# Kernel optimization log

Measured on AMD Instinct MI355X. Metric: run time of the kernel, lower is better.

## Reference

```python
import jax, jax.numpy as jnp
import numpy as np

D_MODEL = 512
NUM_HEADS = 8
D_K = D_MODEL // NUM_HEADS
SCALE = float(np.sqrt(D_K))


def setup_inputs() -> dict:
    key = jax.random.key(0)
    ks = jax.random.split(key, 11)
    B, S, D = 2, 4096, D_MODEL
    std = 1.0 / np.sqrt(D)
    return {
        "query": jax.random.normal(ks[0], (B, S, D), jnp.float32),
        "key": jax.random.normal(ks[1], (B, S, D), jnp.float32),
        "value": jax.random.normal(ks[2], (B, S, D), jnp.float32),
        "w_q": jax.random.normal(ks[3], (D, D), jnp.float32) * std,
        "b_q": jax.random.normal(ks[4], (D,), jnp.float32) * std,
        "w_k": jax.random.normal(ks[5], (D, D), jnp.float32) * std,
        "b_k": jax.random.normal(ks[6], (D,), jnp.float32) * std,
        "w_v": jax.random.normal(ks[7], (D, D), jnp.float32) * std,
        "b_v": jax.random.normal(ks[8], (D,), jnp.float32) * std,
        "w_o": jax.random.normal(ks[9], (D, D), jnp.float32) * std,
        "b_o": jax.random.normal(ks[10], (D,), jnp.float32) * std,
    }


def reference(query, key, value, w_q, b_q, w_k, b_k, w_v, b_v, w_o, b_o):
    B, S, D = query.shape
    H, Dk = NUM_HEADS, D_K
    # Linear projections (torch Linear: x @ W^T + b), split into heads -> [B,H,S,Dk]
    Q = (query @ w_q.T + b_q).reshape(B, S, H, Dk).transpose(0, 2, 1, 3)
    K = (key @ w_k.T + b_k).reshape(B, S, H, Dk).transpose(0, 2, 1, 3)
    V = (value @ w_v.T + b_v).reshape(B, S, H, Dk).transpose(0, 2, 1, 3)
    # [B,H,S,S] attention scores — intentionally materialized like the original
    scores = jnp.einsum("bhqd,bhkd->bhqk", Q, K) / SCALE
    attn = jax.nn.softmax(scores, axis=-1)  # dropout rate 0 in eval baseline
    attended = jnp.einsum("bhqk,bhkd->bhqd", attn, V)
    attended = attended.transpose(0, 2, 1, 3).reshape(B, S, D)
    return attended @ w_o.T + b_o
```

## Files before the change

kernel.cpp:

```cpp
#include <hip/hip_runtime.h>
#include <math.h>

#define D_MODEL 512
#define NHEADS 8
#define DK 64
#define BATCH 2
#define SEQ 4096
#define NSPLIT 2
#define NIT 32
#define ATTN_SCALE 0.18033688011112043f

typedef _Float16 half8 __attribute__((ext_vector_type(8)));
typedef _Float16 half4 __attribute__((ext_vector_type(4)));
typedef __fp16 pkhalf2 __attribute__((ext_vector_type(2)));
typedef float f32x4 __attribute__((ext_vector_type(4)));
typedef float f32x16 __attribute__((ext_vector_type(16)));

union Pk8 { _Float16 h[8]; uint4 u; };
union Pk4 { _Float16 h[4]; uint2 u; };
union Pkz { pkhalf2 h2[2]; uint2 u; };
union Un4 { uint2 u; _Float16 h[4]; };
union PFu { unsigned int u[4]; half8 h8; };

#if __has_builtin(__builtin_amdgcn_exp2f)
#define EXP2F __builtin_amdgcn_exp2f
#else
#define EXP2F exp2f
#endif

#define MFMA16(a, b, c) __builtin_amdgcn_mfma_f32_16x16x32_f16((a), (b), (c), 0, 0, 0)
#define MFMA32(a, b, c) __builtin_amdgcn_mfma_f32_32x32x16_f16((a), (b), (c), 0, 0, 0)

#define PLSWAP(x, y) asm volatile("v_permlane32_swap_b32 %0, %1" : "+v"(x), "+v"(y))

__device__ __forceinline__ unsigned int cvtpk(float a, float b) {
    union { pkhalf2 h; unsigned int u; } u_;
    u_.h = __builtin_amdgcn_cvt_pkrtz(a, b);
    return u_.u;
}

__device__ __forceinline__ void gload_lds16(const _Float16* g, _Float16* l) {
    __builtin_amdgcn_global_load_lds(
        (const __attribute__((address_space(1))) void*)g,
        (__attribute__((address_space(3))) void*)l, 16, 0, 0);
}

#define WBLK 256
__global__ __launch_bounds__(256)
void prep(const float* __restrict__ wq, const float* __restrict__ wk,
          const float* __restrict__ wv, const float* __restrict__ wo,
          _Float16* __restrict__ hq, _Float16* __restrict__ hk,
          _Float16* __restrict__ hv, _Float16* __restrict__ ho) {
    int gid = blockIdx.x;
    const int w = gid / WBLK;
    gid -= w * WBLK;
    const float* src = w == 0 ? wq : (w == 1 ? wk : (w == 2 ? wv : wo));
    _Float16* hi     = w == 0 ? hq : (w == 1 ? hk : (w == 2 ? hv : ho));
    const int i = (gid * 256 + threadIdx.x) * 4;
    float4 v = *(const float4*)(src + i);
    Pkz h;
    h.h2[0] = __builtin_amdgcn_cvt_pkrtz(v.x, v.y);
    h.h2[1] = __builtin_amdgcn_cvt_pkrtz(v.z, v.w);
    *(uint2*)(hi + i) = h.u;
}

__global__ __launch_bounds__(256)
void gemm_qkv(const float* __restrict__ Aq, const float* __restrict__ Ak,
              const float* __restrict__ Av,
              const _Float16* __restrict__ Whq, const _Float16* __restrict__ Whk,
              const _Float16* __restrict__ Whv,
              const float* __restrict__ bq, const float* __restrict__ bk,
              const float* __restrict__ bv,
              _Float16* __restrict__ Qf, _Float16* __restrict__ Kf,
              _Float16* __restrict__ Vtf) {
    const int z = blockIdx.z;
    const float*    A    = z == 0 ? Aq  : (z == 1 ? Ak  : Av);
    const _Float16* Wh   = z == 0 ? Whq : (z == 1 ? Whk : Whv);
    const float*    bias = z == 0 ? bq  : (z == 1 ? bk  : bv);

    __shared__ __align__(16) _Float16 sA[2][128 * 64];
    __shared__ __align__(16) _Float16 sW[2][128 * 64];

    const int t    = threadIdx.x;
    const int lane = t & 63, wave = t >> 6;
    const int col  = lane & 15, quad = lane >> 4;
    const int wm   = (wave & 1) * 64, wn = (wave >> 1) * 64;
    const int m0   = blockIdx.y * 128, n0 = blockIdx.x * 128;

    const int subrow = lane >> 3;
    const int schunk = ((lane & 7) ^ subrow) * 8;

    const float* aBase = A + (size_t)(m0 + wave * 32 + subrow) * 512 + schunk;

    float4 ar[4][2];
    #define LOAD_A(K0)                                                            \
        do {                                                                       \
            _Pragma("unroll")                                                      \
            for (int j = 0; j < 4; ++j) {                                          \
                const float* s = aBase + (size_t)(j * 8) * 512 + (K0);             \
                ar[j][0] = *(const float4*)s;                                      \
                ar[j][1] = *(const float4*)(s + 4);                                \
            }                                                                      \
        } while (0)
    #define WRITE_A(BUF)                                                           \
        do {                                                                       \
            _Pragma("unroll")                                                      \
            for (int j = 0; j < 4; ++j) {                                          \
                uint4 p;                                                           \
                p.x = cvtpk(ar[j][0].x, ar[j][0].y);                               \
                p.y = cvtpk(ar[j][0].z, ar[j][0].w);                               \
                p.z = cvtpk(ar[j][1].x, ar[j][1].y);                               \
                p.w = cvtpk(ar[j][1].z, ar[j][1].w);                               \
                *(uint4*)&sA[BUF][(wave * 32 + j * 8) * 64 + lane * 8] = p;        \
            }                                                                      \
        } while (0)
    #define STAGE_W(K0, BUF)                                                       \
        do {                                                                       \
            _Pragma("unroll")                                                      \
            for (int j = 0; j < 4; ++j) {                                          \
                const int rw = wave * 32 + j * 8;                                  \
                gload_lds16(Wh + (size_t)(n0 + rw + subrow) * 512 + (K0) + schunk, \
                            &sW[BUF][rw * 64]);                                    \
            }                                                                      \
        } while (0)

    f32x4 acc[4][4] = {};

    STAGE_W(0, 0);
    LOAD_A(0);
    WRITE_A(0);

    for (int ck = 0; ck < 8; ++ck) {
        const int cur = ck & 1;
        __syncthreads();
        if (ck + 1 < 8) {
            STAGE_W((ck + 1) * 64, cur ^ 1);
            LOAD_A((ck + 1) * 64);
        }

        #pragma unroll
        for (int kc = 0; kc < 2; ++kc) {
            const int pos = ((kc * 4 + quad) ^ (col & 7)) * 8;
            half8 af[4], wf[4];
            #pragma unroll
            for (int mt = 0; mt < 4; ++mt)
                af[mt] = *(const half8*)&sA[cur][(wm + mt * 16 + col) * 64 + pos];
            #pragma unroll
            for (int nt = 0; nt < 4; ++nt)
                wf[nt] = *(const half8*)&sW[cur][(wn + nt * 16 + col) * 64 + pos];
            #pragma unroll
            for (int mt = 0; mt < 4; ++mt)
                #pragma unroll
                for (int nt = 0; nt < 4; ++nt)
                    acc[mt][nt] = MFMA16(af[mt], wf[nt], acc[mt][nt]);
        }

        if (ck + 1 < 8) WRITE_A(cur ^ 1);
    }

    float bv4[4];
    #pragma unroll
    for (int nt = 0; nt < 4; ++nt) bv4[nt] = bias[n0 + wn + nt * 16 + col];

    if (z < 2) {
        _Float16* Out = z == 0 ? Qf : Kf;
        const float alpha = z == 0 ? ATTN_SCALE : 1.0f;
        #pragma unroll
        for (int mt = 0; mt < 4; ++mt) {
            const int m = m0 + wm + mt * 16 + quad * 4;
            #pragma unroll
            for (int nt = 0; nt < 4; ++nt) {
                const int n = n0 + wn + nt * 16 + col;
                #pragma unroll
                for (int r = 0; r < 4; ++r)
                    Out[(size_t)(m + r) * 512 + n] = (_Float16)((acc[mt][nt][r] + bv4[nt]) * alpha);
            }
        }
    } else {
        #pragma unroll
        for (int mt = 0; mt < 4; ++mt) {
            const int m = m0 + wm + mt * 16 + quad * 4;
            const int b = m >> 12, s = m & (SEQ - 1);
            #pragma unroll
            for (int nt = 0; nt < 4; ++nt) {
                const int n = n0 + wn + nt * 16 + col;
                const int hh = n >> 6, d = n & (DK - 1);
                Pk4 p;
                #pragma unroll
                for (int r = 0; r < 4; ++r)
                    p.h[r] = (_Float16)(acc[mt][nt][r] + bv4[nt]);
                *(uint2*)&Vtf[((size_t)((b * NHEADS + hh) * DK + d)) * SEQ + s] = p.u;
            }
        }
    }
}

__global__ __launch_bounds__(256, 2)
void attn_mfma(const _Float16* __restrict__ Qf, const _Float16* __restrict__ Kf,
               const _Float16* __restrict__ Vtf,
               _Float16* __restrict__ Op0, _Float16* __restrict__ Op1,
               float2* __restrict__ Ml) {
    __shared__ __align__(16) _Float16 sK[2][64 * 64];
    __shared__ __align__(16) _Float16 sV[2][64 * 64];

    const int t    = threadIdx.x;
    const int lane = t & 63;
    const int wave = t >> 6;
    const int l31  = lane & 31;
    const int g    = lane >> 5;

    const int strm = blockIdx.x;
    const int h  = strm & (NHEADS - 1);
    const int z  = strm >> 3;
    const int b  = z >> 1;
    const int sp = z & 1;
    const int q0 = blockIdx.y * 256;
    const int kBase = sp * (SEQ / NSPLIT);

    const size_t rowBase = (size_t)b * SEQ;
    const size_t vBase   = ((size_t)(b * NHEADS + h)) * DK * SEQ;

    const int subrow = lane >> 3;
    const int schunk = ((lane & 7) ^ subrow) * 8;
    const _Float16* kP[2];
    const _Float16* vP[2];
    #pragma unroll
    for (int j = 0; j < 2; ++j) {
        const int rw = wave * 16 + j * 8;
        kP[j] = Kf + (rowBase + kBase + rw + subrow) * 512 + h * 64 + schunk;
        vP[j] = Vtf + vBase + (size_t)(rw + subrow) * SEQ + kBase + schunk;
        gload_lds16(kP[j], &sK[0][rw * 64]);
        gload_lds16(vP[j], &sV[0][rw * 64]);
        kP[j] += 64 * 512;
        vP[j] += 64;
    }

    half8 qf[2][4];
    #pragma unroll
    for (int qt = 0; qt < 2; ++qt)
        #pragma unroll
        for (int kc = 0; kc < 4; ++kc)
            qf[qt][kc] = *(const half8*)(Qf +
                (rowBase + q0 + wave * 64 + qt * 32 + l31) * 512 +
                h * 64 + kc * 16 + g * 8);

    const int rs = l31 & 7;

    float m_r = 0.0f;
    f32x16 nbv = {};
    float l_r[2] = { 0.0f, 0.0f };
    f32x16 of[2][2] = {};

    for (int itp = 0; itp < NIT; itp += 2) {
        #pragma unroll
        for (int cur = 0; cur < 2; ++cur) {
            const int it = itp + cur;
            __syncthreads();
            if (it + 1 < NIT) {
                #pragma unroll
                for (int j = 0; j < 2; ++j) {
                    const int rw = wave * 16 + j * 8;
                    gload_lds16(kP[j], &sK[cur ^ 1][rw * 64]);
                    gload_lds16(vP[j], &sV[cur ^ 1][rw * 64]);
                    kP[j] += 64 * 512;
                    vP[j] += 64;
                }
            }

            #pragma unroll
            for (int kt = 0; kt < 2; ++kt) {
                f32x16 sf0, sf1;
                __builtin_amdgcn_s_setprio(1);
                #pragma unroll
                for (int kc = 0; kc < 4; ++kc) {
                    const int pos = ((kc * 2 + g) ^ rs) * 8;
                    half8 kf = *(const half8*)&sK[cur][(kt * 32 + l31) * 64 + pos];
                    sf0 = MFMA32(kf, qf[0][kc], kc == 0 ? nbv : sf0);
                    sf1 = MFMA32(kf, qf[1][kc], kc == 0 ? nbv : sf1);
                }
                __builtin_amdgcn_s_setprio(0);

                float lrs0 = 0.0f, lrs1 = 0.0f;
                #pragma unroll
                for (int j2 = 0; j2 < 16; ++j2) {
                    sf0[j2] = EXP2F(sf0[j2]);  lrs0 += sf0[j2];
                    sf1[j2] = EXP2F(sf1[j2]);  lrs1 += sf1[j2];
                }
                l_r[0] += lrs0;
                l_r[1] += lrs1;

                PFu pf0[2], pf1[2];
                #define MKPF(P, PF)                                                  \
                    do {                                                             \
                        unsigned int x1 = cvtpk(P[0], P[1]),  x2 = cvtpk(P[2], P[3]);\
                        unsigned int y1 = cvtpk(P[4], P[5]),  y2 = cvtpk(P[6], P[7]);\
                        PLSWAP(x1, y1); PLSWAP(x2, y2);                              \
                        PF[0].u[0] = x1; PF[0].u[1] = x2;                            \
                        PF[0].u[2] = y1; PF[0].u[3] = y2;                            \
                        unsigned int a1 = cvtpk(P[8], P[9]),  a2 = cvtpk(P[10], P[11]);\
                        unsigned int b1 = cvtpk(P[12], P[13]), b2 = cvtpk(P[14], P[15]);\
                        PLSWAP(a1, b1); PLSWAP(a2, b2);                              \
                        PF[1].u[0] = a1; PF[1].u[1] = a2;                            \
                        PF[1].u[2] = b1; PF[1].u[3] = b2;                            \
                    } while (0)
                MKPF(sf0, pf0);
                MKPF(sf1, pf1);
                #undef MKPF

                __builtin_amdgcn_s_setprio(1);
                #pragma unroll
                for (int ks2 = 0; ks2 < 2; ++ks2) {
                    const int ks = kt * 2 + ks2;
                    const int pos = ((ks * 2 + g) ^ rs) * 8;
                    half8 v0 = *(const half8*)&sV[cur][l31 * 64 + pos];
                    half8 v1 = *(const half8*)&sV[cur][(32 + l31) * 64 + pos];
                    of[0][0] = MFMA32(v0, pf0[ks2].h8, of[0][0]);
                    of[0][1] = MFMA32(v1, pf0[ks2].h8, of[0][1]);
                    of[1][0] = MFMA32(v0, pf1[ks2].h8, of[1][0]);
                    of[1][1] = MFMA32(v1, pf1[ks2].h8, of[1][1]);
                }
                __builtin_amdgcn_s_setprio(0);
            }

            if (__any(fmaxf(l_r[0], l_r[1]) > 1048576.0f)) {
                const float al = 0.0009765625f;
                #pragma unroll
                for (int qt = 0; qt < 2; ++qt) {
                    l_r[qt] *= al;
                    #pragma unroll
                    for (int j2 = 0; j2 < 16; ++j2) {
                        of[qt][0][j2] *= al;
                        of[qt][1][j2] *= al;
                    }
                }
                m_r += 10.0f;
                #pragma unroll
                for (int j2 = 0; j2 < 16; ++j2) nbv[j2] = -m_r;
            }
        }
    }

    _Float16* Opx = sp ? Op1 : Op0;
    #pragma unroll
    for (int qt = 0; qt < 2; ++qt) {
        const float l = l_r[qt] + __shfl_xor(l_r[qt], 32);
        const float inv = 1.0f / l;
        const int q = q0 + wave * 64 + qt * 32 + l31;
        const size_t R = rowBase + q;
        #pragma unroll
        for (int dt = 0; dt < 2; ++dt) {
            #pragma unroll
            for (int m4 = 0; m4 < 4; ++m4) {
                const int d0 = dt * 32 + 8 * m4 + 4 * g;
                Pkz z2;
                z2.h2[0] = __builtin_amdgcn_cvt_pkrtz(of[qt][dt][4 * m4 + 0] * inv,
                                                      of[qt][dt][4 * m4 + 1] * inv);
                z2.h2[1] = __builtin_amdgcn_cvt_pkrtz(of[qt][dt][4 * m4 + 2] * inv,
                                                      of[qt][dt][4 * m4 + 3] * inv);
                *(uint2*)(Opx + R * 512 + h * 64 + d0) = z2.u;
            }
        }
        if (lane < 32)
            Ml[((size_t)sp * BATCH * SEQ + R) * NHEADS + h] = make_float2(m_r, l);
    }
}

__global__ __launch_bounds__(256)
void attn_merge(const _Float16* __restrict__ Op0, const _Float16* __restrict__ Op1,
                const float2* __restrict__ Ml, _Float16* __restrict__ Oh) {
    const int i4 = (blockIdx.x * 256 + threadIdx.x) * 4;
    const int R = i4 >> 9;
    const int c = i4 & 511;
    const int h = c >> 6;

    const float2 ml1 = Ml[(size_t)R * NHEADS + h];
    const float2 ml2 = Ml[(size_t)(BATCH * SEQ) * NHEADS + (size_t)R * NHEADS + h];
    const float m = fmaxf(ml1.x, ml2.x);
    float w1 = EXP2F(ml1.x - m) * ml1.y;
    float w2 = EXP2F(ml2.x - m) * ml2.y;
    const float inv = 1.0f / (w1 + w2);
    w1 *= inv; w2 *= inv;

    Un4 a, bb;
    a.u  = *(const uint2*)(Op0 + (size_t)R * 512 + c);
    bb.u = *(const uint2*)(Op1 + (size_t)R * 512 + c);

    Pkz hh;
    hh.h2[0] = __builtin_amdgcn_cvt_pkrtz(w1 * (float)a.h[0] + w2 * (float)bb.h[0],
                                          w1 * (float)a.h[1] + w2 * (float)bb.h[1]);
    hh.h2[1] = __builtin_amdgcn_cvt_pkrtz(w1 * (float)a.h[2] + w2 * (float)bb.h[2],
                                          w1 * (float)a.h[3] + w2 * (float)bb.h[3]);
    *(uint2*)(Oh + (size_t)R * 512 + c) = hh.u;
}

__global__ __launch_bounds__(256)
void gemm_out(const _Float16* __restrict__ Ah, const _Float16* __restrict__ Wh,
              const float* __restrict__ bias, float* __restrict__ C) {
    __shared__ __align__(16) _Float16 sAh[2][128 * 64];
    __shared__ __align__(16) _Float16 sWh[2][64 * 64];

    const int t    = threadIdx.x;
    const int lane = t & 63, wave = t >> 6;
    const int col  = lane & 15, quad = lane >> 4;
    const int wm   = (wave & 1) * 64, wn = (wave >> 1) * 32;
    const int m0   = blockIdx.y * 128, n0 = blockIdx.x * 64;

    const int subrow = lane >> 3;
    const int schunk = ((lane & 7) ^ subrow) * 8;

    #define STAGE_OUT(K0, BUF)                                                       \
        do {                                                                          \
            _Pragma("unroll")                                                         \
            for (int j = 0; j < 4; ++j) {                                             \
                const int rw = wave * 32 + j * 8;                                     \
                gload_lds16(Ah + (size_t)(m0 + rw + subrow) * 512 + (K0) + schunk,    \
                            &sAh[BUF][rw * 64]);                                      \
            }                                                                         \
            _Pragma("unroll")                                                         \
            for (int j = 0; j < 2; ++j) {                                             \
                const int rw = wave * 16 + j * 8;                                     \
                gload_lds16(Wh + (size_t)(n0 + rw + subrow) * 512 + (K0) + schunk,    \
                            &sWh[BUF][rw * 64]);                                      \
            }                                                                         \
        } while (0)

    f32x4 acc[4][2] = {};

    STAGE_OUT(0, 0);
    for (int ck = 0; ck < 8; ++ck) {
        const int cur = ck & 1;
        __syncthreads();
        if (ck + 1 < 8) STAGE_OUT((ck + 1) * 64, cur ^ 1);

        #pragma unroll
        for (int kc = 0; kc < 2; ++kc) {
            const int pos = ((kc * 4 + quad) ^ (col & 7)) * 8;
            half8 ahf[4], whf[2];
            #pragma unroll
            for (int mt = 0; mt < 4; ++mt)
                ahf[mt] = *(const half8*)&sAh[cur][(wm + mt * 16 + col) * 64 + pos];
            #pragma unroll
            for (int nt = 0; nt < 2; ++nt)
                whf[nt] = *(const half8*)&sWh[cur][(wn + nt * 16 + col) * 64 + pos];
            #pragma unroll
            for (int mt = 0; mt < 4; ++mt)
                #pragma unroll
                for (int nt = 0; nt < 2; ++nt)
                    acc[mt][nt] = MFMA16(ahf[mt], whf[nt], acc[mt][nt]);
        }
    }

    float bv2[2];
    #pragma unroll
    for (int nt = 0; nt < 2; ++nt) bv2[nt] = bias[n0 + wn + nt * 16 + col];

    #pragma unroll
    for (int mt = 0; mt < 4; ++mt) {
        const int m = m0 + wm + mt * 16 + quad * 4;
        #pragma unroll
        for (int nt = 0; nt < 2; ++nt) {
            const int n = n0 + wn + nt * 16 + col;
            #pragma unroll
            for (int r = 0; r < 4; ++r)
                C[(size_t)(m + r) * 512 + n] = acc[mt][nt][r] + bv2[nt];
        }
    }
}

extern "C" void kernel_launch(void* const* d_in, const int* in_sizes, int n_in,
                              void* d_out, int out_size, void* d_ws, size_t ws_size,
                              hipStream_t stream) {
    const float* query = (const float*)d_in[0];
    const float* key   = (const float*)d_in[1];
    const float* value = (const float*)d_in[2];
    const float* w_q   = (const float*)d_in[3];
    const float* b_q   = (const float*)d_in[4];
    const float* w_k   = (const float*)d_in[5];
    const float* b_k   = (const float*)d_in[6];
    const float* w_v   = (const float*)d_in[7];
    const float* b_v   = (const float*)d_in[8];
    const float* w_o   = (const float*)d_in[9];
    const float* b_o   = (const float*)d_in[10];
    float* out = (float*)d_out;

    const int WN = D_MODEL * D_MODEL;
    const size_t plane = (size_t)BATCH * SEQ * D_MODEL;

    _Float16* base = (_Float16*)d_ws;
    _Float16* Aq16 = base;
    _Float16* Ak16 = Aq16 + plane;
    _Float16* Av16 = Ak16 + plane;
    _Float16* whq  = Av16 + plane;
    _Float16* whk  = whq + WN;
    _Float16* whv  = whk + WN;
    _Float16* who  = whv + WN;
    _Float16* Qf   = who + WN;
    _Float16* Kf   = Qf + plane;
    _Float16* Vtf  = Kf + plane;
    _Float16* Op1  = Vtf + plane;
    float2*   Ml   = (float2*)(Op1 + plane);
    _Float16* Oh   = Aq16;
    _Float16* Op0  = Av16;

    dim3 blk(256);

    hipLaunchKernelGGL(prep, dim3(4 * WBLK), blk, 0, stream,
                       w_q, w_k, w_v, w_o, whq, whk, whv, who);

    hipLaunchKernelGGL(gemm_qkv, dim3(D_MODEL / 128, BATCH * SEQ / 128, 3), blk, 0, stream,
                       query, key, value,
                       whq, whk, whv,
                       b_q, b_k, b_v, Qf, Kf, Vtf);

    hipLaunchKernelGGL(attn_mfma, dim3(NHEADS * BATCH * NSPLIT, SEQ / 256), blk, 0, stream,
                       Qf, Kf, Vtf, Op0, Op1, Ml);

    hipLaunchKernelGGL(attn_merge, dim3(BATCH * SEQ * D_MODEL / 4 / 256), blk, 0, stream,
                       Op0, Op1, Ml, Oh);

    hipLaunchKernelGGL(gemm_out, dim3(D_MODEL / 64, BATCH * SEQ / 128), blk, 0, stream,
                       Oh, who, b_o, out);
}
```

Before: 240.1 us.

## Fuse split-K attention merge into attention kernel via intra-block LDS exchange

The two key-halves of the split attention now run as two 4-wave groups inside one 512-thread block instead of separate blocks. The first group writes its normalized partial output and (m,l) stats to shared memory, and the second group merges them and writes the final output directly. This removes the separate merge kernel launch and the global round trip of two partial outputs plus stats. In exchange, blocks are larger with double the LDS, which may lower occupancy, and the merge step serializes the two groups at the end.

Result: no change. 235.8 us (-1.8%).

```diff
diff --git a/kernel.cpp b/kernel.cpp
--- a/kernel.cpp
+++ b/kernel.cpp
@@ -6,7 +6,6 @@
 #define DK 64
 #define BATCH 2
 #define SEQ 4096
-#define NSPLIT 2
 #define NIT 32
 #define ATTN_SCALE 0.18033688011112043f
 
@@ -195,30 +194,31 @@
     }
 }
 
-__global__ __launch_bounds__(256, 2)
+__global__ __launch_bounds__(512)
 void attn_mfma(const _Float16* __restrict__ Qf, const _Float16* __restrict__ Kf,
-               const _Float16* __restrict__ Vtf,
-               _Float16* __restrict__ Op0, _Float16* __restrict__ Op1,
-               float2* __restrict__ Ml) {
-    __shared__ __align__(16) _Float16 sK[2][64 * 64];
-    __shared__ __align__(16) _Float16 sV[2][64 * 64];
+               const _Float16* __restrict__ Vtf, _Float16* __restrict__ Oh) {
+    __shared__ __align__(16) _Float16 sKall[2 * 2 * 64 * 64];
+    __shared__ __align__(16) _Float16 sVall[2 * 2 * 64 * 64];
+    __shared__ float2 sMl[256];
 
     const int t    = threadIdx.x;
     const int lane = t & 63;
     const int wave = t >> 6;
+    const int sp   = wave >> 2;
+    const int w4   = wave & 3;
     const int l31  = lane & 31;
     const int g    = lane >> 5;
 
-    const int strm = blockIdx.x;
-    const int h  = strm & (NHEADS - 1);
-    const int z  = strm >> 3;
-    const int b  = z >> 1;
-    const int sp = z & 1;
+    const int h  = blockIdx.x & (NHEADS - 1);
+    const int b  = blockIdx.x >> 3;
     const int q0 = blockIdx.y * 256;
-    const int kBase = sp * (SEQ / NSPLIT);
+    const int kBase = sp * (SEQ / 2);
 
     const size_t rowBase = (size_t)b * SEQ;
     const size_t vBase   = ((size_t)(b * NHEADS + h)) * DK * SEQ;
+
+    _Float16* sK0 = sKall + sp * 2 * 4096;
+    _Float16* sV0 = sVall + sp * 2 * 4096;
 
     const int subrow = lane >> 3;
     const int schunk = ((lane & 7) ^ subrow) * 8;
@@ -226,11 +226,11 @@
     const _Float16* vP[2];
     #pragma unroll
     for (int j = 0; j < 2; ++j) {
-        const int rw = wave * 16 + j * 8;
+        const int rw = w4 * 16 + j * 8;
         kP[j] = Kf + (rowBase + kBase + rw + subrow) * 512 + h * 64 + schunk;
         vP[j] = Vtf + vBase + (size_t)(rw + subrow) * SEQ + kBase + schunk;
-        gload_lds16(kP[j], &sK[0][rw * 64]);
-        gload_lds16(vP[j], &sV[0][rw * 64]);
+        gload_lds16(kP[j], sK0 + rw * 64);
+        gload_lds16(vP[j], sV0 + rw * 64);
         kP[j] += 64 * 512;
         vP[j] += 64;
     }
@@ -241,7 +241,7 @@
         #pragma unroll
         for (int kc = 0; kc < 4; ++kc)
             qf[qt][kc] = *(const half8*)(Qf +
-                (rowBase + q0 + wave * 64 + qt * 32 + l31) * 512 +
+                (rowBase + q0 + w4 * 64 + qt * 32 + l31) * 512 +
                 h * 64 + kc * 16 + g * 8);
 
     const int rs = l31 & 7;
@@ -255,13 +255,15 @@
         #pragma unroll
         for (int cur = 0; cur < 2; ++cur) {
             const int it = itp + cur;
+            _Float16* sK = sK0 + cur * 4096;
+            _Float16* sV = sV0 + cur * 4096;
             __syncthreads();
             if (it + 1 < NIT) {
                 #pragma unroll
                 for (int j = 0; j < 2; ++j) {
-                    const int rw = wave * 16 + j * 8;
-                    gload_lds16(kP[j], &sK[cur ^ 1][rw * 64]);
-                    gload_lds16(vP[j], &sV[cur ^ 1][rw * 64]);
+                    const int rw = w4 * 16 + j * 8;
+                    gload_lds16(kP[j], sK0 + (cur ^ 1) * 4096 + rw * 64);
+                    gload_lds16(vP[j], sV0 + (cur ^ 1) * 4096 + rw * 64);
                     kP[j] += 64 * 512;
                     vP[j] += 64;
                 }
@@ -274,7 +276,7 @@
                 #pragma unroll
                 for (int kc = 0; kc < 4; ++kc) {
                     const int pos = ((kc * 2 + g) ^ rs) * 8;
-                    half8 kf = *(const half8*)&sK[cur][(kt * 32 + l31) * 64 + pos];
+                    half8 kf = *(const half8*)&sK[(kt * 32 + l31) * 64 + pos];
                     sf0 = MFMA32(kf, qf[0][kc], kc == 0 ? nbv : sf0);
                     sf1 = MFMA32(kf, qf[1][kc], kc == 0 ? nbv : sf1);
                 }
@@ -312,8 +314,8 @@
                 for (int ks2 = 0; ks2 < 2; ++ks2) {
                     const int ks = kt * 2 + ks2;
                     const int pos = ((ks * 2 + g) ^ rs) * 8;
-                    half8 v0 = *(const half8*)&sV[cur][l31 * 64 + pos];
-                    half8 v1 = *(const half8*)&sV[cur][(32 + l31) * 64 + pos];
+                    half8 v0 = *(const half8*)&sV[l31 * 64 + pos];
+                    half8 v1 = *(const half8*)&sV[(32 + l31) * 64 + pos];
                     of[0][0] = MFMA32(v0, pf0[ks2].h8, of[0][0]);
                     of[0][1] = MFMA32(v1, pf0[ks2].h8, of[0][1]);
                     of[1][0] = MFMA32(v0, pf1[ks2].h8, of[1][0]);
@@ -340,57 +342,66 @@
         }
     }
 
-    _Float16* Opx = sp ? Op1 : Op0;
-    #pragma unroll
-    for (int qt = 0; qt < 2; ++qt) {
-        const float l = l_r[qt] + __shfl_xor(l_r[qt], 32);
-        const float inv = 1.0f / l;
-        const int q = q0 + wave * 64 + qt * 32 + l31;
-        const size_t R = rowBase + q;
-        #pragma unroll
-        for (int dt = 0; dt < 2; ++dt) {
-            #pragma unroll
-            for (int m4 = 0; m4 < 4; ++m4) {
-                const int d0 = dt * 32 + 8 * m4 + 4 * g;
-                Pkz z2;
-                z2.h2[0] = __builtin_amdgcn_cvt_pkrtz(of[qt][dt][4 * m4 + 0] * inv,
-                                                      of[qt][dt][4 * m4 + 1] * inv);
-                z2.h2[1] = __builtin_amdgcn_cvt_pkrtz(of[qt][dt][4 * m4 + 2] * inv,
-                                                      of[qt][dt][4 * m4 + 3] * inv);
-                *(uint2*)(Opx + R * 512 + h * 64 + d0) = z2.u;
-            }
-        }
-        if (lane < 32)
-            Ml[((size_t)sp * BATCH * SEQ + R) * NHEADS + h] = make_float2(m_r, l);
-    }
-}
-
-__global__ __launch_bounds__(256)
-void attn_merge(const _Float16* __restrict__ Op0, const _Float16* __restrict__ Op1,
-                const float2* __restrict__ Ml, _Float16* __restrict__ Oh) {
-    const int i4 = (blockIdx.x * 256 + threadIdx.x) * 4;
-    const int R = i4 >> 9;
-    const int c = i4 & 511;
-    const int h = c >> 6;
-
-    const float2 ml1 = Ml[(size_t)R * NHEADS + h];
-    const float2 ml2 = Ml[(size_t)(BATCH * SEQ) * NHEADS + (size_t)R * NHEADS + h];
-    const float m = fmaxf(ml1.x, ml2.x);
-    float w1 = EXP2F(ml1.x - m) * ml1.y;
-    float w2 = EXP2F(ml2.x - m) * ml2.y;
-    const float inv = 1.0f / (w1 + w2);
-    w1 *= inv; w2 *= inv;
-
-    Un4 a, bb;
-    a.u  = *(const uint2*)(Op0 + (size_t)R * 512 + c);
-    bb.u = *(const uint2*)(Op1 + (size_t)R * 512 + c);
-
-    Pkz hh;
-    hh.h2[0] = __builtin_amdgcn_cvt_pkrtz(w1 * (float)a.h[0] + w2 * (float)bb.h[0],
-                                          w1 * (float)a.h[1] + w2 * (float)bb.h[1]);
-    hh.h2[1] = __builtin_amdgcn_cvt_pkrtz(w1 * (float)a.h[2] + w2 * (float)bb.h[2],
-                                          w1 * (float)a.h[3] + w2 * (float)bb.h[3]);
-    *(uint2*)(Oh + (size_t)R * 512 + c) = hh.u;
+    __syncthreads();
+    _Float16* sOex = sKall;
+
+    if (sp == 0) {
+        #pragma unroll
+        for (int qt = 0; qt < 2; ++qt) {
+            const float l = l_r[qt] + __shfl_xor(l_r[qt], 32);
+            const float inv = 1.0f / l;
+            const int ql = w4 * 64 + qt * 32 + l31;
+            #pragma unroll
+            for (int dt = 0; dt < 2; ++dt) {
+                #pragma unroll
+                for (int m4 = 0; m4 < 4; ++m4) {
+                    const int d0 = dt * 32 + 8 * m4 + 4 * g;
+                    const int s = (d0 >> 2) ^ ((ql & 7) << 1);
+                    Pkz z2;
+                    z2.h2[0] = __builtin_amdgcn_cvt_pkrtz(of[qt][dt][4 * m4 + 0] * inv,
+                                                          of[qt][dt][4 * m4 + 1] * inv);
+                    z2.h2[1] = __builtin_amdgcn_cvt_pkrtz(of[qt][dt][4 * m4 + 2] * inv,
+                                                          of[qt][dt][4 * m4 + 3] * inv);
+                    *(uint2*)&sOex[ql * 64 + s * 4] = z2.u;
+                }
+            }
+            if (lane < 32) sMl[ql] = make_float2(m_r, l);
+        }
+    }
+    __syncthreads();
+    if (sp == 1) {
+        #pragma unroll
+        for (int qt = 0; qt < 2; ++qt) {
+            const float lB = l_r[qt] + __shfl_xor(l_r[qt], 32);
+            const int ql = w4 * 64 + qt * 32 + l31;
+            const float2 mlA = sMl[ql];
+            const float m = fmaxf(mlA.x, m_r);
+            float wA = EXP2F(mlA.x - m) * mlA.y;
+            float wB = EXP2F(m_r - m) * lB;
+            const float inv = 1.0f / (wA + wB);
+            wA *= inv;
+            const float wBn = wB * inv / lB;
+            const size_t R = rowBase + q0 + ql;
+            #pragma unroll
+            for (int dt = 0; dt < 2; ++dt) {
+                #pragma unroll
+                for (int m4 = 0; m4 < 4; ++m4) {
+                    const int d0 = dt * 32 + 8 * m4 + 4 * g;
+                    const int s = (d0 >> 2) ^ ((ql & 7) << 1);
+                    Un4 oa;
+                    oa.u = *(const uint2*)&sOex[ql * 64 + s * 4];
+                    Pkz z2;
+                    z2.h2[0] = __builtin_amdgcn_cvt_pkrtz(
+                        wA * (float)oa.h[0] + wBn * of[qt][dt][4 * m4 + 0],
+                        wA * (float)oa.h[1] + wBn * of[qt][dt][4 * m4 + 1]);
+                    z2.h2[1] = __builtin_amdgcn_cvt_pkrtz(
+                        wA * (float)oa.h[2] + wBn * of[qt][dt][4 * m4 + 2],
+                        wA * (float)oa.h[3] + wBn * of[qt][dt][4 * m4 + 3]);
+                    *(uint2*)(Oh + R * 512 + h * 64 + d0) = z2.u;
+                }
+            }
+        }
+    }
 }
 
 __global__ __launch_bounds__(256)
@@ -487,20 +498,14 @@
     const size_t plane = (size_t)BATCH * SEQ * D_MODEL;
 
     _Float16* base = (_Float16*)d_ws;
-    _Float16* Aq16 = base;
-    _Float16* Ak16 = Aq16 + plane;
-    _Float16* Av16 = Ak16 + plane;
-    _Float16* whq  = Av16 + plane;
+    _Float16* Oh   = base;
+    _Float16* whq  = Oh + plane;
     _Float16* whk  = whq + WN;
     _Float16* whv  = whk + WN;
     _Float16* who  = whv + WN;
     _Float16* Qf   = who + WN;
     _Float16* Kf   = Qf + plane;
     _Float16* Vtf  = Kf + plane;
-    _Float16* Op1  = Vtf + plane;
-    float2*   Ml   = (float2*)(Op1 + plane);
-    _Float16* Oh   = Aq16;
-    _Float16* Op0  = Av16;
 
     dim3 blk(256);
 
@@ -512,11 +517,8 @@
                        whq, whk, whv,
                        b_q, b_k, b_v, Qf, Kf, Vtf);
 
-    hipLaunchKernelGGL(attn_mfma, dim3(NHEADS * BATCH * NSPLIT, SEQ / 256), blk, 0, stream,
-                       Qf, Kf, Vtf, Op0, Op1, Ml);
-
-    hipLaunchKernelGGL(attn_merge, dim3(BATCH * SEQ * D_MODEL / 4 / 256), blk, 0, stream,
-                       Op0, Op1, Ml, Oh);
+    hipLaunchKernelGGL(attn_mfma, dim3(NHEADS * BATCH, SEQ / 256), dim3(512), 0, stream,
+                       Qf, Kf, Vtf, Oh);
 
     hipLaunchKernelGGL(gemm_out, dim3(D_MODEL / 64, BATCH * SEQ / 128), blk, 0, stream,
                        Oh, who, b_o, out);
```
